# Optimization experiments

Measured on AMD Instinct MI355X. Metric: run time of the kernel, lower is better.

## Reference

```python
import jax, jax.numpy as jnp
import numpy as np

EPS = 1e-12  # matches torch F.normalize default eps

def l2norm(t):
    n = jnp.linalg.norm(t, axis=-1, keepdims=True)
    return t / jnp.maximum(n, EPS)

def rotate_half(x):
    # '... (j d) -> ... j d' with j=2: split into two halves, return cat(-x2, x1)
    x1, x2 = jnp.split(x, 2, axis=-1)
    return jnp.concatenate((-x2, x1), axis=-1)

def rotary_freqs(seq_len, dim):
    inv_freq = 1.0 / (10000.0 ** (jnp.arange(0, dim, 2, dtype=jnp.float32) / dim))
    seq = jnp.arange(seq_len, dtype=jnp.float32)
    freqs = seq[:, None] * inv_freq[None, :]          # [n, d/2]
    emb = jnp.concatenate((freqs, freqs), axis=-1)    # [n, d]
    return emb[None, None]                            # [1, 1, n, d]

def apply_rotary_pos_emb(t, freqs):
    # rot_dim == dim_head here, so the pass-through slice is empty
    return t * jnp.cos(freqs) + rotate_half(t) * jnp.sin(freqs)

def setup_inputs() -> dict:
    key = jax.random.key(0)
    kq, kk, kv = jax.random.split(key, 3)
    b, h, n, d = 2, 16, 2048, 64
    q = jax.random.normal(kq, (b, h, n, d), dtype=jnp.float32)
    k = jax.random.normal(kk, (b, h, n, d), dtype=jnp.float32)
    v = jax.random.normal(kv, (b, h, n, d), dtype=jnp.float32)
    q_scale = jnp.ones((d,), dtype=jnp.float32)
    k_scale = jnp.ones((d,), dtype=jnp.float32)
    return {"q": q, "k": k, "v": v, "q_scale": q_scale, "k_scale": k_scale}

def reference(q, k, v, q_scale, k_scale):
    b, h, n, d = q.shape
    # QK RMSNorm (l2 normalize + learned per-dim scale)
    q = l2norm(q) * q_scale
    k = l2norm(k) * k_scale
    # rotary position embedding (always applied in the source module)
    freqs = rotary_freqs(n, d)
    q = apply_rotary_pos_emb(q, freqs)
    k = apply_rotary_pos_emb(k, freqs)
    # attention: explicit scores -> softmax -> values
    scale = d ** -0.5
    sim = jnp.einsum('bhid,bhjd->bhij', q, k) * scale
    attn = jax.nn.softmax(sim, axis=-1)
    out = jnp.einsum('bhij,bhjd->bhid', attn, v)
    # 'b h n d -> b n (h d)'
    return out.transpose(0, 2, 1, 3).reshape(b, n, h * d)
```

## Files before the change

kernel.cpp:

```cpp
#include <hip/hip_runtime.h>
#include <math.h>

#define BH   32
#define NSEQ 2048
#define DH   64
#define NH   16
#define LOG2E 1.44269504088896f

typedef _Float16 f16x8 __attribute__((ext_vector_type(8)));
typedef __fp16   fp16x2 __attribute__((ext_vector_type(2)));
typedef _Float16 half2v __attribute__((ext_vector_type(2)));
typedef float    f32x16v __attribute__((ext_vector_type(16)));
typedef unsigned uint2v __attribute__((ext_vector_type(2)));

#if __has_builtin(__builtin_amdgcn_exp2f)
#define EXP2F(x) __builtin_amdgcn_exp2f(x)
#else
#define EXP2F(x) exp2f(x)
#endif

static __device__ __forceinline__ unsigned pkrtz(float a, float b) {
    fp16x2 r = __builtin_amdgcn_cvt_pkrtz(a, b);
    return __builtin_bit_cast(unsigned, r);
}
static __device__ __forceinline__ unsigned packh_rne(float a, float b) {
    union { _Float16 h[2]; unsigned u; } x;
    x.h[0] = (_Float16)a; x.h[1] = (_Float16)b;
    return x.u;
}

static __device__ __forceinline__ float2 rope_cs(int pos, int p) {
    float invf_rev = EXP2F(-(float)p * (13.287712379549449f / 32.0f)) * 0.15915494309189535f;
    float rev = (float)pos * invf_rev;
    float fr = rev - floorf(rev);
    float th = fr * 6.283185307179586f;
    return make_float2(__cosf(th), __sinf(th));
}

__global__ __launch_bounds__(256) void prep_all(
    const float* __restrict__ q, const float* __restrict__ k, const float* __restrict__ v,
    const float* __restrict__ qs, const float* __restrict__ ksc,
    unsigned* __restrict__ qh, unsigned* __restrict__ kh, unsigned* __restrict__ vt2) {
    const int bid = blockIdx.x;
    const int t = threadIdx.x;
    if (bid < 16384) {
        const bool isq = bid < 8192;
        const float* in = isq ? q : k;
        const float* sc = isq ? qs : ksc;
        const float smul = isq ? 0.125f * LOG2E : 1.0f;
        const int sb = bid & 8191;
        const int w = t >> 6, lane = t & 63;
        const int c = lane & 31, hfr = lane >> 5;
        const int row = sb * 8 + w * 2 + hfr;
        float2 x2 = *(const float2*)(in + (size_t)row * DH + 2 * c);
        float ss = x2.x * x2.x + x2.y * x2.y;
        #pragma unroll
        for (int off = 16; off > 0; off >>= 1) ss += __shfl_xor(ss, off);
        float inv = 1.0f / fmaxf(sqrtf(ss), 1e-12f);
        float2 s2 = *(const float2*)(sc + 2 * c);
        float t0 = x2.x * inv * s2.x;
        float t1 = x2.y * inv * s2.y;
        float p0 = __shfl_xor(t0, 16);
        float p1 = __shfl_xor(t1, 16);
        float r0 = (c < 16) ? -p0 : p0;
        float r1 = (c < 16) ? -p1 : p1;
        int pos = row & (NSEQ - 1);
        int pp = (2 * c) & 31;
        float2 cs0 = rope_cs(pos, pp);
        float2 cs1 = rope_cs(pos, pp + 1);
        float o0 = (t0 * cs0.x + r0 * cs0.y) * smul;
        float o1 = (t1 * cs1.x + r1 * cs1.y) * smul;
        unsigned val = packh_rne(o0, o1);
        if (isq) {
            qh[row * 32 + c] = val;
        } else {
            const int rloc = row & (NSEQ - 1);
            const unsigned idx = (unsigned)((rloc >> 5) * 1024 + (c >> 3) * 256
                               + ((c >> 2) & 1) * 128 + (rloc & 31) * 4 + (c & 3));
            kh[(size_t)(row >> 11) * 65536 + idx] = val;
        }
    } else {
        const int sb = bid - 16384;
        const int kt = sb & 31, bh = sb >> 5;
        __shared__ float Lv[64 * 68];
        #pragma unroll
        for (int i = 0; i < 4; ++i) {
            int chunk = t + 256 * i;
            int r = chunk >> 4, fg = chunk & 15;
            *(float4*)&Lv[r * 68 + fg * 4] =
                *(const float4*)(v + ((size_t)bh * NSEQ + kt * 64 + r) * DH + fg * 4);
        }
        __syncthreads();
        const int d = t & 63, kg = t >> 6;
        unsigned u[8];
        #pragma unroll
        for (int j = 0; j < 8; ++j) {
            int ky = kg * 16 + 2 * j;
            u[j] = pkrtz(Lv[ky * 68 + d], Lv[(ky + 1) * 68 + d]);
        }
        const int rh = d >> 5, cc = d & 31;
        unsigned* dst = vt2 + (size_t)bh * 65536
                      + (size_t)((kt * 4 + kg) * 2 + rh) * 256 + cc * 4;
        *(uint4*)(dst)       = make_uint4(u[0], u[1], u[2], u[3]);
        *(uint4*)(dst + 128) = make_uint4(u[4], u[5], u[6], u[7]);
    }
}

static __device__ __forceinline__ f16x8 ld8(const unsigned* p) {
    return *(const f16x8*)p;
}

static __device__ __forceinline__ void load_k(f16x8 (&kd)[4], const unsigned* p) {
    #pragma unroll
    for (int ks = 0; ks < 4; ++ks) kd[ks] = ld8(p + ks * 256);
}
static __device__ __forceinline__ void load_v(f16x8 (&vd)[4], const unsigned* p) {
    #pragma unroll
    for (int kk = 0; kk < 2; ++kk)
        #pragma unroll
        for (int rh = 0; rh < 2; ++rh)
            vd[kk * 2 + rh] = ld8(p + kk * 512 + rh * 256);
}

static __device__ __forceinline__ void qk2(
    const f16x8 (&kc)[4], const f16x8 (&qf)[2][4], const f32x16v& z16,
    f32x16v& s0, f32x16v& s1)
{
    __builtin_amdgcn_s_setprio(1);
    s0 = __builtin_amdgcn_mfma_f32_32x32x16_f16(kc[0], qf[0][0], z16, 0, 0, 0);
    s1 = __builtin_amdgcn_mfma_f32_32x32x16_f16(kc[0], qf[1][0], z16, 0, 0, 0);
    #pragma unroll
    for (int ks = 1; ks < 4; ++ks) {
        s0 = __builtin_amdgcn_mfma_f32_32x32x16_f16(kc[ks], qf[0][ks], s0, 0, 0, 0);
        s1 = __builtin_amdgcn_mfma_f32_32x32x16_f16(kc[ks], qf[1][ks], s1, 0, 0, 0);
    }
    __builtin_amdgcn_s_setprio(0);
}

static __device__ __forceinline__ void pv_tile(
    f32x16v& s, const f16x8 (&vc)[4], f32x16v (&ot)[2], float& lp, int hf)
{
    #pragma unroll
    for (int r = 0; r < 16; ++r) s[r] = EXP2F(s[r]);
    #pragma unroll
    for (int kk = 0; kk < 2; ++kk) {
        unsigned P01 = pkrtz(s[kk * 8 + 0], s[kk * 8 + 1]);
        unsigned P23 = pkrtz(s[kk * 8 + 2], s[kk * 8 + 3]);
        unsigned P45 = pkrtz(s[kk * 8 + 4], s[kk * 8 + 5]);
        unsigned P67 = pkrtz(s[kk * 8 + 6], s[kk * 8 + 7]);
#if __has_builtin(__builtin_amdgcn_fdot2)
        const half2v one2 = {(_Float16)1.0f, (_Float16)1.0f};
        lp = __builtin_amdgcn_fdot2(__builtin_bit_cast(half2v, P01), one2, lp, false);
        lp = __builtin_amdgcn_fdot2(__builtin_bit_cast(half2v, P23), one2, lp, false);
        lp = __builtin_amdgcn_fdot2(__builtin_bit_cast(half2v, P45), one2, lp, false);
        lp = __builtin_amdgcn_fdot2(__builtin_bit_cast(half2v, P67), one2, lp, false);
#else
        #pragma unroll
        for (int r = 0; r < 8; ++r) lp += s[kk * 8 + r];
#endif
        union { unsigned u[4]; f16x8 v; } B;
#if __has_builtin(__builtin_amdgcn_permlane32_swap)
        uint2v r02 = __builtin_amdgcn_permlane32_swap(P01, P45, 0, 0);
        uint2v r13 = __builtin_amdgcn_permlane32_swap(P23, P67, 0, 0);
        B.u[0] = r02[0]; B.u[1] = r13[0]; B.u[2] = r02[1]; B.u[3] = r13[1];
#else
        unsigned x01 = (unsigned)__shfl_xor((int)P01, 32);
        unsigned x23 = (unsigned)__shfl_xor((int)P23, 32);
        unsigned x45 = (unsigned)__shfl_xor((int)P45, 32);
        unsigned x67 = (unsigned)__shfl_xor((int)P67, 32);
        B.u[0] = hf ? x45 : P01;
        B.u[1] = hf ? x67 : P23;
        B.u[2] = hf ? P45 : x01;
        B.u[3] = hf ? P67 : x23;
#endif
        __builtin_amdgcn_s_setprio(1);
        ot[0] = __builtin_amdgcn_mfma_f32_32x32x16_f16(vc[kk * 2 + 0], B.v, ot[0], 0, 0, 0);
        ot[1] = __builtin_amdgcn_mfma_f32_32x32x16_f16(vc[kk * 2 + 1], B.v, ot[1], 0, 0, 0);
        __builtin_amdgcn_s_setprio(0);
    }
}

static __device__ __forceinline__ void smpv2(
    f32x16v& s0, f32x16v& s1, const f16x8 (&vc)[4],
    f32x16v (&o)[2][2], float (&lp)[2], int hf)
{
    pv_tile(s0, vc, o[0], lp[0], hf);
    pv_tile(s1, vc, o[1], lp[1], hf);
}

__global__ __launch_bounds__(256, 2) void attn_kernel(
    const unsigned* __restrict__ qh, const unsigned* __restrict__ kf,
    const unsigned* __restrict__ vf, float* __restrict__ out) {

    __shared__ float Lred[128 * 33];

    const int flat = (blockIdx.x & 7) * 64 + (blockIdx.x >> 3);
    const int bh = flat >> 4, qb = flat & 15;

    const int tid = threadIdx.x;
    const int w = tid >> 6, lane = tid & 63;
    const int c = lane & 31, hf = lane >> 5;
    const int qhw = w & 1;
    const int khw = w >> 1;

    const _Float16* qbase = (const _Float16*)qh + ((size_t)bh * NSEQ + qb * 128) * DH;
    f16x8 qf[2][4];
    #pragma unroll
    for (int t = 0; t < 2; ++t)
        #pragma unroll
        for (int ks = 0; ks < 4; ++ks)
            qf[t][ks] = *(const f16x8*)(qbase + (t * 64 + qhw * 32 + c) * DH + ks * 16 + hf * 8);

    const unsigned* kfb = kf + (size_t)bh * 65536 + khw * 1024 + lane * 4;
    const unsigned* vfb = vf + (size_t)bh * 65536 + khw * 1024 + lane * 4;

    f32x16v z16;
    #pragma unroll
    for (int r = 0; r < 16; ++r) z16[r] = 0.f;

    f32x16v o[2][2];
    #pragma unroll
    for (int t = 0; t < 2; ++t)
        #pragma unroll
        for (int mt = 0; mt < 2; ++mt)
            #pragma unroll
            for (int r = 0; r < 16; ++r) o[t][mt][r] = 0.f;
    float lp[2] = {0.f, 0.f};

    f16x8 kc[4], vc[4];
    f32x16v sA0, sA1, sB0, sB1;

    load_k(kc, kfb);
    load_v(vc, vfb);
    qk2(kc, qf, z16, sA0, sA1);
    load_k(kc, kfb + 2048);

    for (int jt = 0; jt < 32; jt += 2) {
        qk2(kc, qf, z16, sB0, sB1);
        if (jt + 2 < 32) load_k(kc, kfb + (size_t)(jt + 2) * 2048);
        smpv2(sA0, sA1, vc, o, lp, hf);
        load_v(vc, vfb + (size_t)(jt + 1) * 2048);

        if (jt + 2 < 32) {
            qk2(kc, qf, z16, sA0, sA1);
            if (jt + 3 < 32) load_k(kc, kfb + (size_t)(jt + 3) * 2048);
        }
        smpv2(sB0, sB1, vc, o, lp, hf);
        if (jt + 2 < 32) load_v(vc, vfb + (size_t)(jt + 2) * 2048);
    }

    float lw[2];
    #pragma unroll
    for (int t = 0; t < 2; ++t) lw[t] = lp[t] + __shfl_xor(lp[t], 32);

    const int b = bh >> 4, h = bh & 15;
    #pragma unroll
    for (int t = 0; t < 2; ++t) {
        if (t) __syncthreads();
        if (w >= 2) {
            const int base = ((w - 2) * 64 + lane) * 33;
            f32x16v* ov = (t == 0) ? &o[0][0] : &o[1][0];
            #pragma unroll
            for (int mt = 0; mt < 2; ++mt)
                #pragma unroll
                for (int r = 0; r < 16; ++r) Lred[base + mt * 16 + r] = ov[mt][r];
            Lred[base + 32] = lw[t];
        }
        __syncthreads();
        if (w < 2) {
            const int base = (w * 64 + lane) * 33;
            f32x16v* ov = (t == 0) ? &o[0][0] : &o[1][0];
            #pragma unroll
            for (int mt = 0; mt < 2; ++mt)
                #pragma unroll
                for (int r = 0; r < 16; ++r) ov[mt][r] += Lred[base + mt * 16 + r];
            float invl = 1.0f / (lw[t] + Lred[base + 32]);
            const int pos = qb * 128 + t * 64 + w * 32 + c;
            float* obase = out + ((size_t)b * NSEQ + pos) * (NH * DH) + h * DH;
            #pragma unroll
            for (int mt = 0; mt < 2; ++mt)
                #pragma unroll
                for (int g = 0; g < 4; ++g) {
                    float4 r4 = make_float4(ov[mt][g * 4 + 0] * invl, ov[mt][g * 4 + 1] * invl,
                                            ov[mt][g * 4 + 2] * invl, ov[mt][g * 4 + 3] * invl);
                    *(float4*)(obase + mt * 32 + g * 8 + hf * 4) = r4;
                }
        }
    }
}

extern "C" void kernel_launch(void* const* d_in, const int* in_sizes, int n_in,
                              void* d_out, int out_size, void* d_ws, size_t ws_size,
                              hipStream_t stream) {
    const float* q  = (const float*)d_in[0];
    const float* k  = (const float*)d_in[1];
    const float* v  = (const float*)d_in[2];
    const float* qs = (const float*)d_in[3];
    const float* ks = (const float*)d_in[4];
    float* outp = (float*)d_out;

    unsigned* qh  = (unsigned*)d_ws;
    unsigned* kh  = qh + (size_t)BH * NSEQ * 32;
    unsigned* vt2 = kh + (size_t)BH * NSEQ * 32;

    prep_all<<<17408, 256, 0, stream>>>(q, k, v, qs, ks, qh, kh, vt2);
    attn_kernel<<<512, 256, 0, stream>>>(qh, kh, vt2, outp);
}
```

Before: 140.8 us.

## Precompute RoPE table, split row-sum chains, stagger KV tile start per block

Adds a small kernel that precomputes a cos/sin table per position, so prep_all reads it instead of evaluating exp2/sin/cos per element. The attention kernel splits the fdot2 row-sum accumulation into two independent chains to shorten the dependency chain. It also rotates the starting K/V tile per block so concurrent blocks touch different memory regions. The change costs an extra kernel launch and some workspace, and the rotated loop now issues one redundant wrapped load at the end.

Result: no change. 142.5 us (+1.2%).

```diff
diff --git a/kernel.cpp b/kernel.cpp
--- a/kernel.cpp
+++ b/kernel.cpp
@@ -37,9 +37,18 @@
     return make_float2(__cosf(th), __sinf(th));
 }
 
+__global__ __launch_bounds__(256) void rope_tab_kernel(float4* __restrict__ tab) {
+    const int id = blockIdx.x * 256 + threadIdx.x;
+    const int pos = id >> 4, j = id & 15;
+    float2 a = rope_cs(pos, 2 * j);
+    float2 b = rope_cs(pos, 2 * j + 1);
+    tab[id] = make_float4(a.x, a.y, b.x, b.y);
+}
+
 __global__ __launch_bounds__(256) void prep_all(
     const float* __restrict__ q, const float* __restrict__ k, const float* __restrict__ v,
     const float* __restrict__ qs, const float* __restrict__ ksc,
+    const float4* __restrict__ tab,
     unsigned* __restrict__ qh, unsigned* __restrict__ kh, unsigned* __restrict__ vt2) {
     const int bid = blockIdx.x;
     const int t = threadIdx.x;
@@ -52,6 +61,8 @@
         const int w = t >> 6, lane = t & 63;
         const int c = lane & 31, hfr = lane >> 5;
         const int row = sb * 8 + w * 2 + hfr;
+        const int pos = row & (NSEQ - 1);
+        const float4 cst = tab[(pos << 4) + (c & 15)];
         float2 x2 = *(const float2*)(in + (size_t)row * DH + 2 * c);
         float ss = x2.x * x2.x + x2.y * x2.y;
         #pragma unroll
@@ -64,12 +75,8 @@
         float p1 = __shfl_xor(t1, 16);
         float r0 = (c < 16) ? -p0 : p0;
         float r1 = (c < 16) ? -p1 : p1;
-        int pos = row & (NSEQ - 1);
-        int pp = (2 * c) & 31;
-        float2 cs0 = rope_cs(pos, pp);
-        float2 cs1 = rope_cs(pos, pp + 1);
-        float o0 = (t0 * cs0.x + r0 * cs0.y) * smul;
-        float o1 = (t1 * cs1.x + r1 * cs1.y) * smul;
+        float o0 = (t0 * cst.x + r0 * cst.y) * smul;
+        float o1 = (t1 * cst.z + r1 * cst.w) * smul;
         unsigned val = packh_rne(o0, o1);
         if (isq) {
             qh[row * 32 + c] = val;
@@ -138,7 +145,7 @@
 }
 
 static __device__ __forceinline__ void pv_tile(
-    f32x16v& s, const f16x8 (&vc)[4], f32x16v (&ot)[2], float& lp, int hf)
+    f32x16v& s, const f16x8 (&vc)[4], f32x16v (&ot)[2], float (&lp2)[2], int hf)
 {
     #pragma unroll
     for (int r = 0; r < 16; ++r) s[r] = EXP2F(s[r]);
@@ -150,13 +157,13 @@
         unsigned P67 = pkrtz(s[kk * 8 + 6], s[kk * 8 + 7]);
 #if __has_builtin(__builtin_amdgcn_fdot2)
         const half2v one2 = {(_Float16)1.0f, (_Float16)1.0f};
-        lp = __builtin_amdgcn_fdot2(__builtin_bit_cast(half2v, P01), one2, lp, false);
-        lp = __builtin_amdgcn_fdot2(__builtin_bit_cast(half2v, P23), one2, lp, false);
-        lp = __builtin_amdgcn_fdot2(__builtin_bit_cast(half2v, P45), one2, lp, false);
-        lp = __builtin_amdgcn_fdot2(__builtin_bit_cast(half2v, P67), one2, lp, false);
+        lp2[0] = __builtin_amdgcn_fdot2(__builtin_bit_cast(half2v, P01), one2, lp2[0], false);
+        lp2[1] = __builtin_amdgcn_fdot2(__builtin_bit_cast(half2v, P23), one2, lp2[1], false);
+        lp2[0] = __builtin_amdgcn_fdot2(__builtin_bit_cast(half2v, P45), one2, lp2[0], false);
+        lp2[1] = __builtin_amdgcn_fdot2(__builtin_bit_cast(half2v, P67), one2, lp2[1], false);
 #else
         #pragma unroll
-        for (int r = 0; r < 8; ++r) lp += s[kk * 8 + r];
+        for (int r = 0; r < 8; ++r) lp2[r & 1] += s[kk * 8 + r];
 #endif
         union { unsigned u[4]; f16x8 v; } B;
 #if __has_builtin(__builtin_amdgcn_permlane32_swap)
@@ -182,7 +189,7 @@
 
 static __device__ __forceinline__ void smpv2(
     f32x16v& s0, f32x16v& s1, const f16x8 (&vc)[4],
-    f32x16v (&o)[2][2], float (&lp)[2], int hf)
+    f32x16v (&o)[2][2], float (&lp)[2][2], int hf)
 {
     pv_tile(s0, vc, o[0], lp[0], hf);
     pv_tile(s1, vc, o[1], lp[1], hf);
@@ -203,6 +210,9 @@
     const int qhw = w & 1;
     const int khw = w >> 1;
 
+    const int st = (blockIdx.x & 3) * 8;
+#define TOFF(j) ((size_t)((st + (j)) & 31) * 2048)
+
     const _Float16* qbase = (const _Float16*)qh + ((size_t)bh * NSEQ + qb * 128) * DH;
     f16x8 qf[2][4];
     #pragma unroll
@@ -225,33 +235,37 @@
         for (int mt = 0; mt < 2; ++mt)
             #pragma unroll
             for (int r = 0; r < 16; ++r) o[t][mt][r] = 0.f;
-    float lp[2] = {0.f, 0.f};
+    float lp[2][2] = {{0.f, 0.f}, {0.f, 0.f}};
 
     f16x8 kc[4], vc[4];
     f32x16v sA0, sA1, sB0, sB1;
 
-    load_k(kc, kfb);
-    load_v(vc, vfb);
+    load_k(kc, kfb + TOFF(0));
+    load_v(vc, vfb + TOFF(0));
     qk2(kc, qf, z16, sA0, sA1);
-    load_k(kc, kfb + 2048);
+    load_k(kc, kfb + TOFF(1));
 
     for (int jt = 0; jt < 32; jt += 2) {
         qk2(kc, qf, z16, sB0, sB1);
-        if (jt + 2 < 32) load_k(kc, kfb + (size_t)(jt + 2) * 2048);
+        load_k(kc, kfb + TOFF(jt + 2));
         smpv2(sA0, sA1, vc, o, lp, hf);
-        load_v(vc, vfb + (size_t)(jt + 1) * 2048);
+        load_v(vc, vfb + TOFF(jt + 1));
 
         if (jt + 2 < 32) {
             qk2(kc, qf, z16, sA0, sA1);
-            if (jt + 3 < 32) load_k(kc, kfb + (size_t)(jt + 3) * 2048);
+            load_k(kc, kfb + TOFF(jt + 3));
         }
         smpv2(sB0, sB1, vc, o, lp, hf);
-        if (jt + 2 < 32) load_v(vc, vfb + (size_t)(jt + 2) * 2048);
-    }
+        load_v(vc, vfb + TOFF(jt + 2));
+    }
+#undef TOFF
 
     float lw[2];
     #pragma unroll
-    for (int t = 0; t < 2; ++t) lw[t] = lp[t] + __shfl_xor(lp[t], 32);
+    for (int t = 0; t < 2; ++t) {
+        lw[t] = lp[t][0] + lp[t][1];
+        lw[t] += __shfl_xor(lw[t], 32);
+    }
 
     const int b = bh >> 4, h = bh & 15;
     #pragma unroll
@@ -302,7 +316,9 @@
     unsigned* qh  = (unsigned*)d_ws;
     unsigned* kh  = qh + (size_t)BH * NSEQ * 32;
     unsigned* vt2 = kh + (size_t)BH * NSEQ * 32;
-
-    prep_all<<<17408, 256, 0, stream>>>(q, k, v, qs, ks, qh, kh, vt2);
+    float4*   tab = (float4*)(vt2 + (size_t)BH * NSEQ * 32);
+
+    rope_tab_kernel<<<128, 256, 0, stream>>>(tab);
+    prep_all<<<17408, 256, 0, stream>>>(q, k, v, qs, ks, tab, qh, kh, vt2);
     attn_kernel<<<512, 256, 0, stream>>>(qh, kh, vt2, outp);
 }
```
